# Kernel optimization log

Measured on AMD Instinct MI355X. Metric: run time of the kernel, lower is better.

## Reference

```python
import jax, jax.numpy as jnp
import numpy as np

B, C, H, W = 8192, 2048, 2, 2
CR = C // 16
EPS = 1e-5

def setup_inputs() -> dict:
    key = jax.random.key(0)
    ks = jax.random.split(key, 8)
    x = jax.random.normal(ks[0], (B, C, H, W), dtype=jnp.float32)
    gamma = jax.random.normal(ks[1], (C,), dtype=jnp.float32) * 0.1 + 1.0
    beta = jax.random.normal(ks[2], (C,), dtype=jnp.float32) * 0.1
    mean = jax.random.normal(ks[3], (C,), dtype=jnp.float32) * 0.1
    var = jax.random.uniform(ks[4], (C,), dtype=jnp.float32, minval=0.5, maxval=1.5)
    w1 = jax.random.normal(ks[5], (CR, C), dtype=jnp.float32) * (1.0 / np.sqrt(C))
    b1 = jnp.zeros((CR,), dtype=jnp.float32)
    w2 = jax.random.normal(ks[6], (C, CR), dtype=jnp.float32) * (1.0 / np.sqrt(CR))
    b2 = jnp.zeros((C,), dtype=jnp.float32)
    return {"x": x, "gamma": gamma, "beta": beta, "mean": mean, "var": var,
            "w1": w1, "b1": b1, "w2": w2, "b2": b2}

def reference(x, gamma, beta, mean, var, w1, b1, w2, b2):
    # BatchNorm (inference form) + ReLU, over [B,C,H,W]
    inv = gamma * jax.lax.rsqrt(var + EPS)           # [C]
    xn = jax.nn.relu(x * inv[None, :, None, None]
                     + (beta - mean * inv)[None, :, None, None])
    # global average pool -> [B, C]
    p = jnp.mean(xn, axis=(2, 3))
    # two 1x1 convs on [B,C,1,1] == channel MLP
    h = jax.nn.relu(jnp.einsum('bc,rc->br', p, w1) + b1)   # [B, C/16]
    g = jax.nn.sigmoid(jnp.einsum('br,cr->bc', h, w2) + b2) # [B, C]
    # repeat(1,1,2,2) then in-place add == broadcast add over 2x2 spatial
    return x + g[:, :, None, None]
```

## Files before the change

kernel.cpp:

```cpp
#include <hip/hip_runtime.h>


typedef unsigned short u16;
typedef unsigned int u32;
typedef short short8 __attribute__((ext_vector_type(8)));
typedef __bf16 bf16x8 __attribute__((ext_vector_type(8)));
typedef unsigned short ushort4v __attribute__((ext_vector_type(4)));
typedef float floatx4 __attribute__((ext_vector_type(4)));
typedef float floatx2 __attribute__((ext_vector_type(2)));

#define C_CH 2048
#define NB 16
#define THREADS 512
#define PROW 2056
#define HROW 136

__device__ __forceinline__ float bf2f(u16 u) {
    u32 v = ((u32)u) << 16;
    return __builtin_bit_cast(float, v);
}
__device__ __forceinline__ u16 f2bf(float f) {
    u32 v = __builtin_bit_cast(u32, f);
    v = (v + 0x7FFFu + ((v >> 16) & 1u)) >> 16;
    return (u16)v;
}
__device__ __forceinline__ bf16x8 ld8(const u16* p) {
    short8 s = *(const short8*)p;
    return __builtin_bit_cast(bf16x8, s);
}
__device__ __forceinline__ bf16x8 cvt8(floatx4 a, floatx4 b) {
    short8 s;
    s[0] = (short)f2bf(a[0]); s[1] = (short)f2bf(a[1]);
    s[2] = (short)f2bf(a[2]); s[3] = (short)f2bf(a[3]);
    s[4] = (short)f2bf(b[0]); s[5] = (short)f2bf(b[1]);
    s[6] = (short)f2bf(b[2]); s[7] = (short)f2bf(b[3]);
    return __builtin_bit_cast(bf16x8, s);
}
__device__ __forceinline__ bool is_bf16_data(const u16* var_raw) {
    int ok = 1;
    #pragma unroll
    for (int i = 0; i < 8; ++i) {
        u16 u = var_raw[2 * i];
        ok &= (u >= 0x3F00u) && (u <= 0x3FC0u);
    }
    return ok != 0;
}

extern "C" __global__ void __launch_bounds__(THREADS, 4)
se_fused(const void* __restrict__ x_raw,
         const void* __restrict__ gamma_raw,
         const void* __restrict__ beta_raw,
         const void* __restrict__ mean_raw,
         const void* __restrict__ var_raw,
         const void* __restrict__ w1_raw,
         const void* __restrict__ b1_raw,
         const void* __restrict__ w2_raw,
         const void* __restrict__ b2_raw,
         void* __restrict__ out_raw) {
    __shared__ u16 p_lds[NB * PROW];
    __shared__ u16 h_lds[NB * HROW];

    const int tid  = threadIdx.x;
    const int lane = tid & 63;
    const int wv   = tid >> 6;
    const int quad = lane >> 4;
    const int l16  = lane & 15;
    const long b0  = (long)blockIdx.x * NB;

    const bool bf = is_bf16_data((const u16*)var_raw);

    {
        const short8*  x8b = (const short8*)((const u16*)x_raw + b0 * 8192);
        const floatx4* x4f = (const floatx4*)x_raw + b0 * 2048;
        const u16 *gu = (const u16*)gamma_raw, *bu = (const u16*)beta_raw,
                  *mu = (const u16*)mean_raw,  *vu = (const u16*)var_raw;
        const float *gf = (const float*)gamma_raw, *bfp = (const float*)beta_raw,
                    *mf = (const float*)mean_raw,  *vf = (const float*)var_raw;

        for (int i = 0; i < 32; ++i) {
            int idx8 = i * THREADS + tid;
            int e    = idx8 << 3;
            int m    = e >> 13;
            int c0   = (e & 8191) >> 2;
            float xs[8];
            float gm0, gm1, bt0, bt1, mn0, mn1, vr0, vr1;
            if (bf) {
                short8 xv = x8b[idx8];
                #pragma unroll
                for (int j = 0; j < 8; ++j) xs[j] = bf2f((u16)xv[j]);
                u32 t;
                t = *(const u32*)(gu + c0); gm0 = bf2f((u16)t); gm1 = bf2f((u16)(t >> 16));
                t = *(const u32*)(bu + c0); bt0 = bf2f((u16)t); bt1 = bf2f((u16)(t >> 16));
                t = *(const u32*)(mu + c0); mn0 = bf2f((u16)t); mn1 = bf2f((u16)(t >> 16));
                t = *(const u32*)(vu + c0); vr0 = bf2f((u16)t); vr1 = bf2f((u16)(t >> 16));
            } else {
                floatx4 xa = x4f[2 * idx8], xb = x4f[2 * idx8 + 1];
                #pragma unroll
                for (int j = 0; j < 4; ++j) { xs[j] = xa[j]; xs[4 + j] = xb[j]; }
                floatx2 t2;
                t2 = *(const floatx2*)(gf  + c0); gm0 = t2[0]; gm1 = t2[1];
                t2 = *(const floatx2*)(bfp + c0); bt0 = t2[0]; bt1 = t2[1];
                t2 = *(const floatx2*)(mf  + c0); mn0 = t2[0]; mn1 = t2[1];
                t2 = *(const floatx2*)(vf  + c0); vr0 = t2[0]; vr1 = t2[1];
            }
            float inv0 = gm0 * rsqrtf(vr0 + 1e-5f); float bs0 = bt0 - mn0 * inv0;
            float inv1 = gm1 * rsqrtf(vr1 + 1e-5f); float bs1 = bt1 - mn1 * inv1;
            float s0 = 0.f, s1 = 0.f;
            #pragma unroll
            for (int j = 0; j < 4; ++j) s0 += fmaxf(fmaf(xs[j],     inv0, bs0), 0.f);
            #pragma unroll
            for (int j = 0; j < 4; ++j) s1 += fmaxf(fmaf(xs[4 + j], inv1, bs1), 0.f);
            u32 packed = (u32)f2bf(s0 * 0.25f) | ((u32)f2bf(s1 * 0.25f) << 16);
            *(u32*)(&p_lds[m * PROW + c0]) = packed;
        }
    }
    __syncthreads();

    const int rr = (wv << 4) | l16;
    {
        floatx4 acc = {0.f, 0.f, 0.f, 0.f};
        const u16* pp = p_lds + l16 * PROW + (quad << 3);
        if (bf) {
            const u16* w1p = (const u16*)w1_raw + (long)rr * C_CH + (quad << 3);
            #pragma unroll 4
            for (int k0 = 0; k0 < C_CH; k0 += 32)
                acc = __builtin_amdgcn_mfma_f32_16x16x32_bf16(ld8(pp + k0), ld8(w1p + k0), acc, 0, 0, 0);
        } else {
            const float* w1p = (const float*)w1_raw + (long)rr * C_CH + (quad << 3);
            #pragma unroll 2
            for (int k0 = 0; k0 < C_CH; k0 += 32) {
                floatx4 wa = *(const floatx4*)(w1p + k0);
                floatx4 wb = *(const floatx4*)(w1p + k0 + 4);
                acc = __builtin_amdgcn_mfma_f32_16x16x32_bf16(ld8(pp + k0), cvt8(wa, wb), acc, 0, 0, 0);
            }
        }
        float bb = bf ? bf2f(((const u16*)b1_raw)[rr]) : ((const float*)b1_raw)[rr];
        #pragma unroll
        for (int r = 0; r < 4; ++r) {
            int m = (quad << 2) | r;
            h_lds[m * HROW + rr] = f2bf(fmaxf(acc[r] + bb, 0.f));
        }
    }
    __syncthreads();

    bf16x8 af[4];
    #pragma unroll
    for (int kk = 0; kk < 4; ++kk)
        af[kk] = ld8(h_lds + l16 * HROW + (kk << 5) + (quad << 3));

    const ushort4v* x4u = (const ushort4v*)x_raw;
    ushort4v*       o4u = (ushort4v*)out_raw;
    const floatx4*  x4f = (const floatx4*)x_raw;
    floatx4*        o4f = (floatx4*)out_raw;

    for (int i = 0; i < 16; ++i) {
        int c = (wv * 16 + i) * 16 + l16;
        floatx4 a2 = {0.f, 0.f, 0.f, 0.f};
        if (bf) {
            const u16* w2p = (const u16*)w2_raw + (long)c * 128 + (quad << 3);
            #pragma unroll
            for (int kk = 0; kk < 4; ++kk)
                a2 = __builtin_amdgcn_mfma_f32_16x16x32_bf16(af[kk], ld8(w2p + (kk << 5)), a2, 0, 0, 0);
        } else {
            const float* w2p = (const float*)w2_raw + (long)c * 128 + (quad << 3);
            #pragma unroll
            for (int kk = 0; kk < 4; ++kk) {
                floatx4 wa = *(const floatx4*)(w2p + (kk << 5));
                floatx4 wb = *(const floatx4*)(w2p + (kk << 5) + 4);
                a2 = __builtin_amdgcn_mfma_f32_16x16x32_bf16(af[kk], cvt8(wa, wb), a2, 0, 0, 0);
            }
        }
        float zb = bf ? bf2f(((const u16*)b2_raw)[c]) : ((const float*)b2_raw)[c];
        #pragma unroll
        for (int r = 0; r < 4; ++r) {
            int m = (quad << 2) | r;
            float z = a2[r] + zb;
            float g = 1.f / (1.f + __expf(-z));
            long idx = (b0 + m) * 2048 + c;
            if (bf) {
                ushort4v xv = x4u[idx];
                ushort4v ov;
                #pragma unroll
                for (int j = 0; j < 4; ++j) ov[j] = f2bf(bf2f(xv[j]) + g);
                o4u[idx] = ov;
            } else {
                floatx4 xv = x4f[idx];
                floatx4 ov;
                #pragma unroll
                for (int j = 0; j < 4; ++j) ov[j] = xv[j] + g;
                o4f[idx] = ov;
            }
        }
    }
}

extern "C" void kernel_launch(void* const* d_in, const int* in_sizes, int n_in,
                              void* d_out, int out_size, void* d_ws, size_t ws_size,
                              hipStream_t stream) {
    se_fused<<<dim3(8192 / NB), dim3(THREADS), 0, stream>>>(
        d_in[0], d_in[1], d_in[2], d_in[3], d_in[4],
        d_in[5], d_in[6], d_in[7], d_in[8], d_out);
}
```

Baseline: 599.9 us.

## Halve batch per block to 8 and hoist BN params out of pooling loop

Each block now handles 8 batch rows instead of 16, which doubles the grid to 1024 blocks and raises the launch-bounds occupancy hint. The 16-row MFMA tiles now duplicate rows (l16&7), and the upper half of lanes skips the stores. The pooling loop is restructured so each thread owns fixed channel pairs, which lets the BN scale and shift be loaded and computed once rather than per iteration. The cost is that half the MFMA work is wasted, and weights are re-read from cache by twice as many blocks.

```diff
diff --git a/kernel.cpp b/kernel.cpp
--- a/kernel.cpp
+++ b/kernel.cpp
@@ -10,7 +10,7 @@
 typedef float floatx2 __attribute__((ext_vector_type(2)));
 
 #define C_CH 2048
-#define NB 16
+#define NB 8
 #define THREADS 512
 #define PROW 2056
 #define HROW 136
@@ -46,7 +46,7 @@
     return ok != 0;
 }
 
-extern "C" __global__ void __launch_bounds__(THREADS, 4)
+extern "C" __global__ void __launch_bounds__(THREADS, 8)
 se_fused(const void* __restrict__ x_raw,
          const void* __restrict__ gamma_raw,
          const void* __restrict__ beta_raw,
@@ -70,48 +70,80 @@
     const bool bf = is_bf16_data((const u16*)var_raw);
 
     {
-        const short8*  x8b = (const short8*)((const u16*)x_raw + b0 * 8192);
-        const floatx4* x4f = (const floatx4*)x_raw + b0 * 2048;
-        const u16 *gu = (const u16*)gamma_raw, *bu = (const u16*)beta_raw,
-                  *mu = (const u16*)mean_raw,  *vu = (const u16*)var_raw;
-        const float *gf = (const float*)gamma_raw, *bfp = (const float*)beta_raw,
-                    *mf = (const float*)mean_raw,  *vf = (const float*)var_raw;
-
-        for (int i = 0; i < 32; ++i) {
-            int idx8 = i * THREADS + tid;
-            int e    = idx8 << 3;
-            int m    = e >> 13;
-            int c0   = (e & 8191) >> 2;
-            float xs[8];
-            float gm0, gm1, bt0, bt1, mn0, mn1, vr0, vr1;
-            if (bf) {
-                short8 xv = x8b[idx8];
+        const int cA = tid << 1;
+        const int cB = cA + 1024;
+        float gmA0, gmA1, btA0, btA1, mnA0, mnA1, vrA0, vrA1;
+        float gmB0, gmB1, btB0, btB1, mnB0, mnB1, vrB0, vrB1;
+        if (bf) {
+            const u16 *gu = (const u16*)gamma_raw, *bu = (const u16*)beta_raw,
+                      *mu = (const u16*)mean_raw,  *vu = (const u16*)var_raw;
+            u32 t;
+            t = *(const u32*)(gu + cA); gmA0 = bf2f((u16)t); gmA1 = bf2f((u16)(t >> 16));
+            t = *(const u32*)(bu + cA); btA0 = bf2f((u16)t); btA1 = bf2f((u16)(t >> 16));
+            t = *(const u32*)(mu + cA); mnA0 = bf2f((u16)t); mnA1 = bf2f((u16)(t >> 16));
+            t = *(const u32*)(vu + cA); vrA0 = bf2f((u16)t); vrA1 = bf2f((u16)(t >> 16));
+            t = *(const u32*)(gu + cB); gmB0 = bf2f((u16)t); gmB1 = bf2f((u16)(t >> 16));
+            t = *(const u32*)(bu + cB); btB0 = bf2f((u16)t); btB1 = bf2f((u16)(t >> 16));
+            t = *(const u32*)(mu + cB); mnB0 = bf2f((u16)t); mnB1 = bf2f((u16)(t >> 16));
+            t = *(const u32*)(vu + cB); vrB0 = bf2f((u16)t); vrB1 = bf2f((u16)(t >> 16));
+        } else {
+            const float *gf = (const float*)gamma_raw, *bfp = (const float*)beta_raw,
+                        *mf = (const float*)mean_raw,  *vf = (const float*)var_raw;
+            floatx2 t2;
+            t2 = *(const floatx2*)(gf  + cA); gmA0 = t2[0]; gmA1 = t2[1];
+            t2 = *(const floatx2*)(bfp + cA); btA0 = t2[0]; btA1 = t2[1];
+            t2 = *(const floatx2*)(mf  + cA); mnA0 = t2[0]; mnA1 = t2[1];
+            t2 = *(const floatx2*)(vf  + cA); vrA0 = t2[0]; vrA1 = t2[1];
+            t2 = *(const floatx2*)(gf  + cB); gmB0 = t2[0]; gmB1 = t2[1];
+            t2 = *(const floatx2*)(bfp + cB); btB0 = t2[0]; btB1 = t2[1];
+            t2 = *(const floatx2*)(mf  + cB); mnB0 = t2[0]; mnB1 = t2[1];
+            t2 = *(const floatx2*)(vf  + cB); vrB0 = t2[0]; vrB1 = t2[1];
+        }
+        const float invA0 = gmA0 * rsqrtf(vrA0 + 1e-5f), bsA0 = btA0 - mnA0 * invA0;
+        const float invA1 = gmA1 * rsqrtf(vrA1 + 1e-5f), bsA1 = btA1 - mnA1 * invA1;
+        const float invB0 = gmB0 * rsqrtf(vrB0 + 1e-5f), bsB0 = btB0 - mnB0 * invB0;
+        const float invB1 = gmB1 * rsqrtf(vrB1 + 1e-5f), bsB1 = btB1 - mnB1 * invB1;
+
+        if (bf) {
+            const short8* x8b = (const short8*)((const u16*)x_raw + b0 * 8192);
+            #pragma unroll 2
+            for (int m = 0; m < NB; ++m) {
+                short8 xa = x8b[(m << 10) + tid];
+                short8 xb = x8b[(m << 10) + 512 + tid];
+                float sA0 = 0.f, sA1 = 0.f, sB0 = 0.f, sB1 = 0.f;
                 #pragma unroll
-                for (int j = 0; j < 8; ++j) xs[j] = bf2f((u16)xv[j]);
-                u32 t;
-                t = *(const u32*)(gu + c0); gm0 = bf2f((u16)t); gm1 = bf2f((u16)(t >> 16));
-                t = *(const u32*)(bu + c0); bt0 = bf2f((u16)t); bt1 = bf2f((u16)(t >> 16));
-                t = *(const u32*)(mu + c0); mn0 = bf2f((u16)t); mn1 = bf2f((u16)(t >> 16));
-                t = *(const u32*)(vu + c0); vr0 = bf2f((u16)t); vr1 = bf2f((u16)(t >> 16));
-            } else {
-                floatx4 xa = x4f[2 * idx8], xb = x4f[2 * idx8 + 1];
+                for (int j = 0; j < 4; ++j) {
+                    sA0 += fmaxf(fmaf(bf2f((u16)xa[j]),     invA0, bsA0), 0.f);
+                    sA1 += fmaxf(fmaf(bf2f((u16)xa[4 + j]), invA1, bsA1), 0.f);
+                    sB0 += fmaxf(fmaf(bf2f((u16)xb[j]),     invB0, bsB0), 0.f);
+                    sB1 += fmaxf(fmaf(bf2f((u16)xb[4 + j]), invB1, bsB1), 0.f);
+                }
+                *(u32*)(&p_lds[m * PROW + cA]) =
+                    (u32)f2bf(sA0 * 0.25f) | ((u32)f2bf(sA1 * 0.25f) << 16);
+                *(u32*)(&p_lds[m * PROW + cB]) =
+                    (u32)f2bf(sB0 * 0.25f) | ((u32)f2bf(sB1 * 0.25f) << 16);
+            }
+        } else {
+            const floatx4* x4f = (const floatx4*)x_raw + b0 * 2048;
+            #pragma unroll 2
+            for (int m = 0; m < NB; ++m) {
+                int ia = (m << 10) + tid;
+                int ib = ia + 512;
+                floatx4 a0 = x4f[2 * ia], a1 = x4f[2 * ia + 1];
+                floatx4 c0 = x4f[2 * ib], c1 = x4f[2 * ib + 1];
+                float sA0 = 0.f, sA1 = 0.f, sB0 = 0.f, sB1 = 0.f;
                 #pragma unroll
-                for (int j = 0; j < 4; ++j) { xs[j] = xa[j]; xs[4 + j] = xb[j]; }
-                floatx2 t2;
-                t2 = *(const floatx2*)(gf  + c0); gm0 = t2[0]; gm1 = t2[1];
-                t2 = *(const floatx2*)(bfp + c0); bt0 = t2[0]; bt1 = t2[1];
-                t2 = *(const floatx2*)(mf  + c0); mn0 = t2[0]; mn1 = t2[1];
-                t2 = *(const floatx2*)(vf  + c0); vr0 = t2[0]; vr1 = t2[1];
-            }
-            float inv0 = gm0 * rsqrtf(vr0 + 1e-5f); float bs0 = bt0 - mn0 * inv0;
-            float inv1 = gm1 * rsqrtf(vr1 + 1e-5f); float bs1 = bt1 - mn1 * inv1;
-            float s0 = 0.f, s1 = 0.f;
-            #pragma unroll
-            for (int j = 0; j < 4; ++j) s0 += fmaxf(fmaf(xs[j],     inv0, bs0), 0.f);
-            #pragma unroll
-            for (int j = 0; j < 4; ++j) s1 += fmaxf(fmaf(xs[4 + j], inv1, bs1), 0.f);
-            u32 packed = (u32)f2bf(s0 * 0.25f) | ((u32)f2bf(s1 * 0.25f) << 16);
-            *(u32*)(&p_lds[m * PROW + c0]) = packed;
+                for (int j = 0; j < 4; ++j) {
+                    sA0 += fmaxf(fmaf(a0[j], invA0, bsA0), 0.f);
+                    sA1 += fmaxf(fmaf(a1[j], invA1, bsA1), 0.f);
+                    sB0 += fmaxf(fmaf(c0[j], invB0, bsB0), 0.f);
+                    sB1 += fmaxf(fmaf(c1[j], invB1, bsB1), 0.f);
+                }
+                *(u32*)(&p_lds[m * PROW + cA]) =
+                    (u32)f2bf(sA0 * 0.25f) | ((u32)f2bf(sA1 * 0.25f) << 16);
+                *(u32*)(&p_lds[m * PROW + cB]) =
+                    (u32)f2bf(sB0 * 0.25f) | ((u32)f2bf(sB1 * 0.25f) << 16);
+            }
         }
     }
     __syncthreads();
@@ -119,7 +151,7 @@
     const int rr = (wv << 4) | l16;
     {
         floatx4 acc = {0.f, 0.f, 0.f, 0.f};
-        const u16* pp = p_lds + l16 * PROW + (quad << 3);
+        const u16* pp = p_lds + (l16 & 7) * PROW + (quad << 3);
         if (bf) {
             const u16* w1p = (const u16*)w1_raw + (long)rr * C_CH + (quad << 3);
             #pragma unroll 4
@@ -135,10 +167,12 @@
             }
         }
         float bb = bf ? bf2f(((const u16*)b1_raw)[rr]) : ((const float*)b1_raw)[rr];
-        #pragma unroll
-        for (int r = 0; r < 4; ++r) {
-            int m = (quad << 2) | r;
-            h_lds[m * HROW + rr] = f2bf(fmaxf(acc[r] + bb, 0.f));
+        if (quad < 2) {
+            #pragma unroll
+            for (int r = 0; r < 4; ++r) {
+                int m = (quad << 2) | r;
+                h_lds[m * HROW + rr] = f2bf(fmaxf(acc[r] + bb, 0.f));
+            }
         }
     }
     __syncthreads();
@@ -146,7 +180,7 @@
     bf16x8 af[4];
     #pragma unroll
     for (int kk = 0; kk < 4; ++kk)
-        af[kk] = ld8(h_lds + l16 * HROW + (kk << 5) + (quad << 3));
+        af[kk] = ld8(h_lds + (l16 & 7) * HROW + (kk << 5) + (quad << 3));
 
     const ushort4v* x4u = (const ushort4v*)x_raw;
     ushort4v*       o4u = (ushort4v*)out_raw;
@@ -171,24 +205,26 @@
             }
         }
         float zb = bf ? bf2f(((const u16*)b2_raw)[c]) : ((const float*)b2_raw)[c];
-        #pragma unroll
-        for (int r = 0; r < 4; ++r) {
-            int m = (quad << 2) | r;
-            float z = a2[r] + zb;
-            float g = 1.f / (1.f + __expf(-z));
-            long idx = (b0 + m) * 2048 + c;
-            if (bf) {
-                ushort4v xv = x4u[idx];
-                ushort4v ov;
-                #pragma unroll
-                for (int j = 0; j < 4; ++j) ov[j] = f2bf(bf2f(xv[j]) + g);
-                o4u[idx] = ov;
-            } else {
-                floatx4 xv = x4f[idx];
-                floatx4 ov;
-                #pragma unroll
-                for (int j = 0; j < 4; ++j) ov[j] = xv[j] + g;
-                o4f[idx] = ov;
+        if (quad < 2) {
+            #pragma unroll
+            for (int r = 0; r < 4; ++r) {
+                int m = (quad << 2) | r;
+                float z = a2[r] + zb;
+                float g = 1.f / (1.f + __expf(-z));
+                long idx = (b0 + m) * 2048 + c;
+                if (bf) {
+                    ushort4v xv = x4u[idx];
+                    ushort4v ov;
+                    #pragma unroll
+                    for (int j = 0; j < 4; ++j) ov[j] = f2bf(bf2f(xv[j]) + g);
+                    o4u[idx] = ov;
+                } else {
+                    floatx4 xv = x4f[idx];
+                    floatx4 ov;
+                    #pragma unroll
+                    for (int j = 0; j < 4; ++j) ov[j] = xv[j] + g;
+                    o4f[idx] = ov;
+                }
             }
         }
     }
```

Result: slower. 674.3 us (+12.4%).
